# Kernel tuning notes

Hardware: AMD Instinct MI355X
Metric: run time of the kernel (lower is better)

## Reference

```python
import jax, jax.numpy as jnp
import numpy as np

EPS = 1e-5  # torch BatchNorm1d default eps


def _bn(x, gamma, beta):
    # Training-mode BatchNorm1d: per-batch mean/var (biased), affine.
    mu = jnp.mean(x, axis=0)
    var = jnp.var(x, axis=0)
    return (x - mu) * jax.lax.rsqrt(var + EPS) * gamma + beta


def _trunk(x, layers):
    # For each hidden layer: Tanh(Linear(BatchNorm(x)))
    for (W, b, g, be) in layers:
        x = jnp.tanh(_bn(x, g, be) @ W + b)
    return x


def setup_inputs() -> dict:
    key = jax.random.key(0)
    ks = jax.random.split(key, 16)
    B, N, D = 4096, 8192, 1024
    dims = [D, 1024, 512, 256]
    inp = {
        "x": jax.random.normal(ks[0], (B, D), dtype=jnp.float32),
        "x_n": jax.random.normal(ks[1], (N, D), dtype=jnp.float32),
        "y_n": jax.random.uniform(ks[2], (N, 1), dtype=jnp.float32),
    }
    for i in range(3):
        fan_in, fan_out = dims[i], dims[i + 1]
        bound = 1.0 / np.sqrt(fan_in)
        inp[f"W{i+1}"] = jax.random.uniform(ks[3 + 4 * i], (fan_in, fan_out), minval=-bound, maxval=bound, dtype=jnp.float32)
        inp[f"b{i+1}"] = jax.random.uniform(ks[4 + 4 * i], (fan_out,), minval=-bound, maxval=bound, dtype=jnp.float32)
        inp[f"g{i+1}"] = jnp.ones((fan_in,), dtype=jnp.float32)
        inp[f"beta{i+1}"] = jnp.zeros((fan_in,), dtype=jnp.float32)
    return inp


def reference(x, x_n, y_n,
              W1, b1, g1, beta1,
              W2, b2, g2, beta2,
              W3, b3, g3, beta3):
    layers = [(W1, b1, g1, beta1), (W2, b2, g2, beta2), (W3, b3, g3, beta3)]
    q = _trunk(x, layers)      # [B, 256]
    k = _trunk(x_n, layers)    # [N, 256]
    # l2 similarity: negative squared euclidean distance, via GEMM.
    # sim[i,j] = -||q_i - k_j||^2 = 2 q_i.k_j - ||q_i||^2 - ||k_j||^2
    q2 = jnp.sum(q * q, axis=1, keepdims=True)          # [B,1]
    k2 = jnp.sum(k * k, axis=1)                          # [N]
    sim = 2.0 * (q @ k.T) - q2 - k2[None, :]             # [B,N]
    # x != x_n (different shapes) => train=False, no diagonal masking.
    scores = jax.nn.softmax(sim, axis=1)
    out = jnp.clip(scores @ y_n, 0.0, 1.0)               # [B,1]
    return jnp.squeeze(out, axis=1)                      # [B]
```

## Files before the change

### kernel.cpp

```cpp
#include <hip/hip_runtime.h>
#include <math.h>
#include <stdint.h>


typedef __attribute__((ext_vector_type(8))) _Float16 half8;
typedef __attribute__((ext_vector_type(4))) _Float16 half4;
typedef __attribute__((ext_vector_type(4))) float floatx4;

#define L2E  1.4426950408889634f
#define SCALE2 2.8853901817f

__device__ __forceinline__ float fast_tanh(float x) {
    float ax = fabsf(x);
    float e  = __expf(-2.0f * ax);
    float r  = (1.0f - e) / (1.0f + e);
    return copysignf(r, x);
}
__device__ __forceinline__ void gload16(const void* g, void* l) {
    __builtin_amdgcn_global_load_lds(
        (__attribute__((address_space(1))) void*)(uintptr_t)(g),
        (__attribute__((address_space(3))) void*)(unsigned int)(uintptr_t)(l),
        16, 0, 0);
}

__global__ __launch_bounds__(256) void tof16_stats_all(
        const float* __restrict__ xn, const float* __restrict__ x,
        _Float16* __restrict__ xnh, _Float16* __restrict__ xh,
        float* __restrict__ cs0, float* __restrict__ cq0,
        float* __restrict__ cs3, float* __restrict__ cq3) {
    const float* in; _Float16* out; float *cs, *cq; int r0;
    if (blockIdx.x < 256) { in = xn; out = xnh; cs = cs0; cq = cq0; r0 = blockIdx.x * 32; }
    else                  { in = x;  out = xh;  cs = cs3; cq = cq3; r0 = (blockIdx.x - 256) * 32; }
    const int c = threadIdx.x * 4;
    float s0 = 0.f, s1 = 0.f, s2 = 0.f, s3 = 0.f;
    float q0 = 0.f, q1 = 0.f, q2 = 0.f, q3 = 0.f;
    for (int r = r0; r < r0 + 32; ++r) {
        float4 v = *(const float4*)&in[(size_t)r * 1024 + c];
        half4 h;
        h[0] = (_Float16)v.x; h[1] = (_Float16)v.y;
        h[2] = (_Float16)v.z; h[3] = (_Float16)v.w;
        *(half4*)&out[(size_t)r * 1024 + c] = h;
        s0 += v.x; q0 += v.x * v.x;
        s1 += v.y; q1 += v.y * v.y;
        s2 += v.z; q2 += v.z * v.z;
        s3 += v.w; q3 += v.w * v.w;
    }
    atomicAdd(&cs[c + 0], s0); atomicAdd(&cq[c + 0], q0);
    atomicAdd(&cs[c + 1], s1); atomicAdd(&cq[c + 1], q1);
    atomicAdd(&cs[c + 2], s2); atomicAdd(&cq[c + 2], q2);
    atomicAdd(&cs[c + 3], s3); atomicAdd(&cq[c + 3], q3);
}

__global__ __launch_bounds__(256) void wprep2(
        const float* __restrict__ W, const float* __restrict__ g,
        const float* __restrict__ beta,
        const float* __restrict__ csK, const float* __restrict__ cqK, float invRK,
        _Float16* __restrict__ WTk, float* __restrict__ baccK,
        const float* __restrict__ csQ, const float* __restrict__ cqQ, float invRQ,
        _Float16* __restrict__ WTq, float* __restrict__ baccQ,
        int C, int F) {
    const int z = blockIdx.z;
    const float* cs = z ? csQ : csK;
    const float* cq = z ? cqQ : cqK;
    const float invR = z ? invRQ : invRK;
    _Float16* WT = z ? WTq : WTk;
    float* bacc = z ? baccQ : baccK;

    __shared__ float sv[32], tv[32];
    __shared__ float tile[32][33];
    __shared__ float lds2[8][32];
    const int c0 = blockIdx.y * 32, f0 = blockIdx.x * 32;
    const int tx = threadIdx.x & 31, ty = threadIdx.x >> 5;
    if (ty == 0) {
        int c = c0 + tx;
        float mean = cs[c] * invR;
        float var  = fmaxf(cq[c] * invR - mean * mean, 0.f);
        float s    = g[c] * rsqrtf(var + 1e-5f);
        sv[tx] = s;
        tv[tx] = beta[c] - mean * s;
    }
    __syncthreads();
    float pacc = 0.f;
#pragma unroll
    for (int i = 0; i < 32; i += 8) {
        float w = W[(size_t)(c0 + ty + i) * F + f0 + tx];
        tile[ty + i][tx] = w * sv[ty + i];
        pacc += w * tv[ty + i];
    }
    lds2[ty][tx] = pacc;
    __syncthreads();
#pragma unroll
    for (int i = 0; i < 32; i += 8)
        WT[(size_t)(f0 + ty + i) * C + c0 + tx] = (_Float16)tile[tx][ty + i];
    if (ty == 0) {
        float a = 0.f;
#pragma unroll
        for (int j = 0; j < 8; ++j) a += lds2[j][tx];
        atomicAdd(&bacc[f0 + tx], a);
    }
}

__global__ __launch_bounds__(256, 4) void gemm_tn_tanh(
        const _Float16* __restrict__ Ak, const _Float16* __restrict__ Aq,
        const _Float16* __restrict__ WTk, const _Float16* __restrict__ WTq,
        const float* __restrict__ bias,
        const float* __restrict__ baccK, const float* __restrict__ baccQ,
        _Float16* __restrict__ Yk, _Float16* __restrict__ Yq,
        int K, int F, int smodeK, int smodeQ,
        float* __restrict__ csK, float* __restrict__ cqK,
        float* __restrict__ csQ, float* __restrict__ cqQ,
        float* __restrict__ rowsqK) {
    __shared__ _Float16 As[128 * 64];
    __shared__ _Float16 Bs[128 * 64];
    const int tid = threadIdx.x;
    const int wv = tid >> 6, ln = tid & 63;
    const int quad = ln >> 4, l16 = ln & 15;
    const int wr = wv >> 1, wc = wv & 1;

    const bool isK = blockIdx.x < 64;
    const _Float16* A  = isK ? Ak : Aq;
    const _Float16* WT = isK ? WTk : WTq;
    const float* bacc  = isK ? baccK : baccQ;
    _Float16* Y        = isK ? Yk : Yq;
    const int smode    = isK ? smodeK : smodeQ;
    float* cs = isK ? csK : csQ;
    float* cq = isK ? cqK : cqQ;
    const int i0 = (isK ? blockIdx.x : blockIdx.x - 64) * 128;
    const int f0 = blockIdx.y * 128;

    floatx4 acc[4][4];
#pragma unroll
    for (int a = 0; a < 4; ++a)
#pragma unroll
        for (int b = 0; b < 4; ++b) acc[a][b] = (floatx4)0.f;

    for (int k0 = 0; k0 < K; k0 += 64) {
        const char* Ab = (const char*)(A + (size_t)i0 * K + k0);
        const char* Bb = (const char*)(WT + (size_t)f0 * K + k0);
#pragma unroll
        for (int it = 0; it < 4; ++it) {
            int seg = it * 256 + tid;
            int row = seg >> 3, p = seg & 7;
            int lcol = (p ^ row) & 7;
            gload16(Ab + (size_t)row * (K * 2) + lcol * 16, (char*)As + seg * 16);
        }
#pragma unroll
        for (int it = 0; it < 4; ++it) {
            int seg = it * 256 + tid;
            int row = seg >> 3, p = seg & 7;
            int lcol = (p ^ row) & 7;
            gload16(Bb + (size_t)row * (K * 2) + lcol * 16, (char*)Bs + seg * 16);
        }
        __syncthreads();
#pragma unroll
        for (int kk = 0; kk < 2; ++kk) {
            half8 af[4], bf[4];
#pragma unroll
            for (int t = 0; t < 4; ++t) {
                int ra = wr * 64 + t * 16 + l16;
                int ca = ((kk * 4 + quad) ^ ra) & 7;
                af[t] = *(const half8*)((const char*)As + ra * 128 + ca * 16);
                int rb = wc * 64 + t * 16 + l16;
                int cb = ((kk * 4 + quad) ^ rb) & 7;
                bf[t] = *(const half8*)((const char*)Bs + rb * 128 + cb * 16);
            }
#pragma unroll
            for (int tr = 0; tr < 4; ++tr)
#pragma unroll
                for (int tc = 0; tc < 4; ++tc)
                    acc[tr][tc] = __builtin_amdgcn_mfma_f32_16x16x32_f16(af[tr], bf[tc], acc[tr][tc], 0, 0, 0);
        }
        __syncthreads();
    }
#pragma unroll
    for (int tc = 0; tc < 4; ++tc) {
        int f = f0 + wc * 64 + tc * 16 + l16;
        float bb = bias[f] + bacc[f];
#pragma unroll
        for (int tr = 0; tr < 4; ++tr)
#pragma unroll
            for (int r = 0; r < 4; ++r) {
                int row = i0 + wr * 64 + tr * 16 + quad * 4 + r;
                float v = fast_tanh(acc[tr][tc][r] + bb);
                acc[tr][tc][r] = v;
                Y[(size_t)row * F + f] = (_Float16)v;
            }
    }
    if (smode == 1) {
#pragma unroll
        for (int tc = 0; tc < 4; ++tc) {
            int f = f0 + wc * 64 + tc * 16 + l16;
            float s = 0.f, q = 0.f;
#pragma unroll
            for (int tr = 0; tr < 4; ++tr)
#pragma unroll
                for (int r = 0; r < 4; ++r) {
                    float v = acc[tr][tc][r];
                    s += v; q += v * v;
                }
            s += __shfl_xor(s, 16); q += __shfl_xor(q, 16);
            s += __shfl_xor(s, 32); q += __shfl_xor(q, 32);
            if (quad == 0) {
                atomicAdd(&cs[f], s);
                atomicAdd(&cq[f], q);
            }
        }
    } else if (smode == 2) {
#pragma unroll
        for (int tr = 0; tr < 4; ++tr)
#pragma unroll
            for (int r = 0; r < 4; ++r) {
                float rq = 0.f;
#pragma unroll
                for (int tc = 0; tc < 4; ++tc) {
                    float v = acc[tr][tc][r];
                    rq += v * v;
                }
                rq += __shfl_xor(rq, 1); rq += __shfl_xor(rq, 2);
                rq += __shfl_xor(rq, 4); rq += __shfl_xor(rq, 8);
                if (l16 == 0)
                    atomicAdd(&rowsqK[i0 + wr * 64 + tr * 16 + quad * 4 + r], rq * L2E);
            }
    }
}

__global__ __launch_bounds__(256, 2) void flash_mfma(
        const _Float16* __restrict__ Q, const _Float16* __restrict__ K3,
        const float* __restrict__ k2s, const float* __restrict__ yv,
        float* __restrict__ pm, float* __restrict__ pl, float* __restrict__ po,
        int jlen, int nsplit) {
    __shared__ _Float16 Ts[128 * 256];
    const int tid = threadIdx.x;
    const int wv = tid >> 6, ln = tid & 63;
    const int quad = ln >> 4, l16 = ln & 15;
    const int i0 = blockIdx.x * 128;
    const int jb = blockIdx.y * jlen;
    const int nch = jlen >> 6;

    auto stage64 = [&](const _Float16* src, int bufseg) {
        const char* sb = (const char*)src;
#pragma unroll
        for (int it = 0; it < 8; ++it) {
            int seg = it * 256 + tid;
            int row = seg >> 5, p = seg & 31;
            int lcol = (p & 24) | ((p ^ row) & 7);
            gload16(sb + (size_t)row * 512 + lcol * 16, (char*)Ts + (bufseg + seg) * 16);
        }
    };

    stage64(Q + (size_t)i0 * 256, 0);
    stage64(Q + (size_t)(i0 + 64) * 256, 2048);
    __syncthreads();
    half8 qf[2][8];
#pragma unroll
    for (int tr = 0; tr < 2; ++tr)
#pragma unroll
        for (int k0 = 0; k0 < 8; ++k0) {
            int row = wv * 32 + tr * 16 + l16;
            int c = k0 * 4 + quad;
            int phys = (c & 24) | ((c ^ row) & 7);
            qf[tr][k0] = *(const half8*)((const char*)Ts + row * 512 + phys * 16);
        }
    asm volatile("s_waitcnt lgkmcnt(0)" ::: "memory");
    __syncthreads();

    float mrun[2][4], lrun[2][4], orun[2][4];
#pragma unroll
    for (int tr = 0; tr < 2; ++tr)
#pragma unroll
        for (int r = 0; r < 4; ++r) { mrun[tr][r] = -INFINITY; lrun[tr][r] = 0.f; orun[tr][r] = 0.f; }

    stage64(K3 + (size_t)jb * 256, 0);
    __syncthreads();
    for (int jc = 0; jc < nch; ++jc) {
        const int j0 = jb + jc * 64;
        const int bseg = (jc & 1) * 2048;
        if (jc + 1 < nch) stage64(K3 + (size_t)(j0 + 64) * 256, 2048 - bseg);
        floatx4 acc[2][4];
#pragma unroll
        for (int a = 0; a < 2; ++a)
#pragma unroll
            for (int b = 0; b < 4; ++b) acc[a][b] = (floatx4)0.f;
#pragma unroll
        for (int k0 = 0; k0 < 8; ++k0) {
            half8 kf[4];
#pragma unroll
            for (int tc = 0; tc < 4; ++tc) {
                int row = tc * 16 + l16;
                int c = k0 * 4 + quad;
                int phys = (c & 24) | ((c ^ row) & 7);
                kf[tc] = *(const half8*)((const char*)Ts + bseg * 16 + row * 512 + phys * 16);
            }
#pragma unroll
            for (int tr = 0; tr < 2; ++tr)
#pragma unroll
                for (int tc = 0; tc < 4; ++tc)
                    acc[tr][tc] = __builtin_amdgcn_mfma_f32_16x16x32_f16(qf[tr][k0], kf[tc], acc[tr][tc], 0, 0, 0);
        }
        float k2v[4], yv4[4];
#pragma unroll
        for (int tc = 0; tc < 4; ++tc) {
            int j = j0 + tc * 16 + l16;
            k2v[tc] = k2s[j];
            yv4[tc] = yv[j];
        }
#pragma unroll
        for (int tr = 0; tr < 2; ++tr)
#pragma unroll
            for (int r = 0; r < 4; ++r) {
                float lg[4], mt = -INFINITY;
#pragma unroll
                for (int tc = 0; tc < 4; ++tc) {
                    lg[tc] = SCALE2 * acc[tr][tc][r] - k2v[tc];
                    mt = fmaxf(mt, lg[tc]);
                }
                float mnew = fmaxf(mrun[tr][r], mt);
                float sc = exp2f(mrun[tr][r] - mnew);
                float sp = 0.f, spy = 0.f;
#pragma unroll
                for (int tc = 0; tc < 4; ++tc) {
                    float p = exp2f(lg[tc] - mnew);
                    sp  += p;
                    spy += p * yv4[tc];
                }
                lrun[tr][r] = lrun[tr][r] * sc + sp;
                orun[tr][r] = orun[tr][r] * sc + spy;
                mrun[tr][r] = mnew;
            }
        __syncthreads();
    }
#pragma unroll
    for (int tr = 0; tr < 2; ++tr)
#pragma unroll
        for (int r = 0; r < 4; ++r) {
            float m = mrun[tr][r], l = lrun[tr][r], o = orun[tr][r];
#pragma unroll
            for (int s = 1; s < 16; s <<= 1) {
                float m2 = __shfl_xor(m, s);
                float l2 = __shfl_xor(l, s);
                float o2 = __shfl_xor(o, s);
                float mn = fmaxf(m, m2);
                float a = exp2f(m - mn), b = exp2f(m2 - mn);
                l = l * a + l2 * b;
                o = o * a + o2 * b;
                m = mn;
            }
            if (l16 == 0) {
                int row = i0 + wv * 32 + tr * 16 + quad * 4 + r;
                size_t idx = (size_t)row * nsplit + blockIdx.y;
                pm[idx] = m;
                pl[idx] = l;
                po[idx] = o;
            }
        }
}

__global__ void combine_k(const float* __restrict__ pm, const float* __restrict__ pl,
                          const float* __restrict__ po, float* __restrict__ out,
                          int B, int nsplit) {
    int i = blockIdx.x * blockDim.x + threadIdx.x;
    if (i >= B) return;
    float M = -INFINITY;
    for (int s = 0; s < nsplit; ++s) M = fmaxf(M, pm[(size_t)i * nsplit + s]);
    float L = 0.f, O = 0.f;
    for (int s = 0; s < nsplit; ++s) {
        float w = exp2f(pm[(size_t)i * nsplit + s] - M);
        L += pl[(size_t)i * nsplit + s] * w;
        O += po[(size_t)i * nsplit + s] * w;
    }
    float r = O / L;
    out[i] = fminf(fmaxf(r, 0.f), 1.f);
}

extern "C" void kernel_launch(void* const* d_in, const int* in_sizes, int n_in,
                              void* d_out, int out_size, void* d_ws, size_t ws_size,
                              hipStream_t stream) {
    const float* x   = (const float*)d_in[0];
    const float* x_n = (const float*)d_in[1];
    const float* y_n = (const float*)d_in[2];
    const float* Wm[3]    = {(const float*)d_in[3],  (const float*)d_in[7],  (const float*)d_in[11]};
    const float* bm[3]    = {(const float*)d_in[4],  (const float*)d_in[8],  (const float*)d_in[12]};
    const float* gm[3]    = {(const float*)d_in[5],  (const float*)d_in[9],  (const float*)d_in[13]};
    const float* betam[3] = {(const float*)d_in[6],  (const float*)d_in[10], (const float*)d_in[14]};
    (void)in_sizes; (void)n_in; (void)out_size; (void)ws_size;

    const int B = 4096, N = 8192;
    const int NSPLIT = 16;
    const size_t M1 = 1024 * 1024;

    _Float16* h0 = (_Float16*)d_ws;
    _Float16* h1 = h0 + 8 * M1;
    _Float16* h2 = h1 + 4 * M1;
    _Float16* h3 = h2 + 8 * M1;
    _Float16* WTk = h3 + 4 * M1;
    _Float16* WTq = WTk + M1;
    float* fb = (float*)(WTq + M1);
    float* csA[6], *cqA[6];
    for (int i = 0; i < 6; ++i) { csA[i] = fb + i * 2048; cqA[i] = fb + i * 2048 + 1024; }
    float* baccK[3], *baccQ[3];
    for (int i = 0; i < 3; ++i) { baccK[i] = fb + 12288 + i * 1024; baccQ[i] = fb + 15360 + i * 1024; }
    float* k2n = fb + 18432;
    const size_t zero_floats = 18432 + 8192;
    float* pm = fb + zero_floats;
    float* pl = pm + (size_t)B * NSPLIT;
    float* po = pl + (size_t)B * NSPLIT;

    _Float16* xnh = h0, *xh = h1;
    _Float16* actAk = h2, *actAq = h3;
    _Float16* actBk = h0, *actBq = h1;
    _Float16* k3 = h2, *q3 = h2 + 2 * M1;

    hipMemsetAsync(fb, 0, zero_floats * sizeof(float), stream);
    tof16_stats_all<<<384, 256, 0, stream>>>(x_n, x, xnh, xh,
                                             csA[0], cqA[0], csA[3], cqA[3]);
    const float invRK = 1.0f / (float)N, invRQ = 1.0f / (float)B;

    wprep2<<<dim3(1024 / 32, 1024 / 32, 2), 256, 0, stream>>>(
        Wm[0], gm[0], betam[0], csA[0], cqA[0], invRK, WTk, baccK[0],
        csA[3], cqA[3], invRQ, WTq, baccQ[0], 1024, 1024);
    gemm_tn_tanh<<<dim3(96, 1024 / 128), 256, 0, stream>>>(
        xnh, xh, WTk, WTq, bm[0], baccK[0], baccQ[0], actAk, actAq,
        1024, 1024, 1, 1, csA[1], cqA[1], csA[4], cqA[4], nullptr);
    wprep2<<<dim3(512 / 32, 1024 / 32, 2), 256, 0, stream>>>(
        Wm[1], gm[1], betam[1], csA[1], cqA[1], invRK, WTk, baccK[1],
        csA[4], cqA[4], invRQ, WTq, baccQ[1], 1024, 512);
    gemm_tn_tanh<<<dim3(96, 512 / 128), 256, 0, stream>>>(
        actAk, actAq, WTk, WTq, bm[1], baccK[1], baccQ[1], actBk, actBq,
        1024, 512, 1, 1, csA[2], cqA[2], csA[5], cqA[5], nullptr);
    wprep2<<<dim3(256 / 32, 512 / 32, 2), 256, 0, stream>>>(
        Wm[2], gm[2], betam[2], csA[2], cqA[2], invRK, WTk, baccK[2],
        csA[5], cqA[5], invRQ, WTq, baccQ[2], 512, 256);
    gemm_tn_tanh<<<dim3(96, 256 / 128), 256, 0, stream>>>(
        actBk, actBq, WTk, WTq, bm[2], baccK[2], baccQ[2], k3, q3,
        512, 256, 2, 0, nullptr, nullptr, nullptr, nullptr, k2n);

    flash_mfma<<<dim3(B / 128, NSPLIT), 256, 0, stream>>>(
        q3, k3, k2n, y_n, pm, pl, po, N / NSPLIT, NSPLIT);
    combine_k<<<B / 256, 256, 0, stream>>>(pm, pl, po, (float*)d_out, B, NSPLIT);
}
```

Baseline: 270.6 us.

## Double-buffer LDS tiles with K-step 32 in trunk GEMM

```diff
diff --git a/kernel.cpp b/kernel.cpp
--- a/kernel.cpp
+++ b/kernel.cpp
@@ -110,8 +110,8 @@
         float* __restrict__ csK, float* __restrict__ cqK,
         float* __restrict__ csQ, float* __restrict__ cqQ,
         float* __restrict__ rowsqK) {
-    __shared__ _Float16 As[128 * 64];
-    __shared__ _Float16 Bs[128 * 64];
+    __shared__ _Float16 As[2][128 * 32];
+    __shared__ _Float16 Bs[2][128 * 32];
     const int tid = threadIdx.x;
     const int wv = tid >> 6, ln = tid & 63;
     const int quad = ln >> 4, l16 = ln & 15;
@@ -128,48 +128,54 @@
     const int i0 = (isK ? blockIdx.x : blockIdx.x - 64) * 128;
     const int f0 = blockIdx.y * 128;
 
+    const size_t ldb = (size_t)K * 2;
+    const char* Abase = (const char*)(A + (size_t)i0 * K);
+    const char* Bbase = (const char*)(WT + (size_t)f0 * K);
+
+    auto stage = [&](const char* src, int kb, char* dst) {
+#pragma unroll
+        for (int it = 0; it < 2; ++it) {
+            int slot = it * 256 + tid;
+            int rgrp = slot >> 4;
+            int segp = (slot >> 2) & 3;
+            int rowi = slot & 3;
+            int row  = rgrp * 4 + rowi;
+            int lseg = (segp ^ rgrp) & 3;
+            gload16(src + (size_t)row * ldb + kb + lseg * 16, dst + slot * 16);
+        }
+    };
+
     floatx4 acc[4][4];
 #pragma unroll
     for (int a = 0; a < 4; ++a)
 #pragma unroll
         for (int b = 0; b < 4; ++b) acc[a][b] = (floatx4)0.f;
 
-    for (int k0 = 0; k0 < K; k0 += 64) {
-        const char* Ab = (const char*)(A + (size_t)i0 * K + k0);
-        const char* Bb = (const char*)(WT + (size_t)f0 * K + k0);
-#pragma unroll
-        for (int it = 0; it < 4; ++it) {
-            int seg = it * 256 + tid;
-            int row = seg >> 3, p = seg & 7;
-            int lcol = (p ^ row) & 7;
-            gload16(Ab + (size_t)row * (K * 2) + lcol * 16, (char*)As + seg * 16);
-        }
-#pragma unroll
-        for (int it = 0; it < 4; ++it) {
-            int seg = it * 256 + tid;
-            int row = seg >> 3, p = seg & 7;
-            int lcol = (p ^ row) & 7;
-            gload16(Bb + (size_t)row * (K * 2) + lcol * 16, (char*)Bs + seg * 16);
-        }
-        __syncthreads();
-#pragma unroll
-        for (int kk = 0; kk < 2; ++kk) {
-            half8 af[4], bf[4];
-#pragma unroll
-            for (int t = 0; t < 4; ++t) {
-                int ra = wr * 64 + t * 16 + l16;
-                int ca = ((kk * 4 + quad) ^ ra) & 7;
-                af[t] = *(const half8*)((const char*)As + ra * 128 + ca * 16);
-                int rb = wc * 64 + t * 16 + l16;
-                int cb = ((kk * 4 + quad) ^ rb) & 7;
-                bf[t] = *(const half8*)((const char*)Bs + rb * 128 + cb * 16);
-            }
-#pragma unroll
-            for (int tr = 0; tr < 4; ++tr)
-#pragma unroll
-                for (int tc = 0; tc < 4; ++tc)
-                    acc[tr][tc] = __builtin_amdgcn_mfma_f32_16x16x32_f16(af[tr], bf[tc], acc[tr][tc], 0, 0, 0);
-        }
+    const int niter = K >> 5;
+    stage(Abase, 0, (char*)As[0]);
+    stage(Bbase, 0, (char*)Bs[0]);
+    __syncthreads();
+    for (int it = 0; it < niter; ++it) {
+        const int cur = it & 1, nxt = cur ^ 1;
+        if (it + 1 < niter) {
+            stage(Abase, (it + 1) * 64, (char*)As[nxt]);
+            stage(Bbase, (it + 1) * 64, (char*)Bs[nxt]);
+        }
+        half8 af[4], bf[4];
+#pragma unroll
+        for (int t = 0; t < 4; ++t) {
+            int ra = wr * 64 + t * 16 + l16;
+            int pa = (quad ^ (ra >> 2)) & 3;
+            af[t] = *(const half8*)((const char*)As[cur] + (ra >> 2) * 256 + pa * 64 + (ra & 3) * 16);
+            int rb = wc * 64 + t * 16 + l16;
+            int pb = (quad ^ (rb >> 2)) & 3;
+            bf[t] = *(const half8*)((const char*)Bs[cur] + (rb >> 2) * 256 + pb * 64 + (rb & 3) * 16);
+        }
+#pragma unroll
+        for (int tr = 0; tr < 4; ++tr)
+#pragma unroll
+            for (int tc = 0; tc < 4; ++tc)
+                acc[tr][tc] = __builtin_amdgcn_mfma_f32_16x16x32_f16(af[tr], bf[tc], acc[tr][tc], 0, 0, 0);
         __syncthreads();
     }
 #pragma unroll
```

New measurement: 301.2 us. 1.11x slower.

## Template trunk GEMM tiles, load A fragments directly from global, prefetch B

Applied to the files above, without the earlier changes.

```diff
diff --git a/kernel.cpp b/kernel.cpp
--- a/kernel.cpp
+++ b/kernel.cpp
@@ -100,7 +100,8 @@
     }
 }
 
-__global__ __launch_bounds__(256, 4) void gemm_tn_tanh(
+template <int BM, int BN, int WC>
+__global__ __launch_bounds__(256, 3) void gemm_tn_tanh(
         const _Float16* __restrict__ Ak, const _Float16* __restrict__ Aq,
         const _Float16* __restrict__ WTk, const _Float16* __restrict__ WTq,
         const float* __restrict__ bias,
@@ -110,14 +111,18 @@
         float* __restrict__ csK, float* __restrict__ cqK,
         float* __restrict__ csQ, float* __restrict__ cqQ,
         float* __restrict__ rowsqK) {
-    __shared__ _Float16 As[128 * 64];
-    __shared__ _Float16 Bs[128 * 64];
+    constexpr int WR = 4 / WC;
+    constexpr int TR = BM / WR / 16;
+    constexpr int TC = BN / WC / 16;
+    __shared__ _Float16 Bs[BN * 64];
     const int tid = threadIdx.x;
     const int wv = tid >> 6, ln = tid & 63;
     const int quad = ln >> 4, l16 = ln & 15;
-    const int wr = wv >> 1, wc = wv & 1;
-
-    const bool isK = blockIdx.x < 64;
+    const int wr = (WC == 1) ? wv : (wv >> 1);
+    const int wc = (WC == 1) ? 0  : (wv & 1);
+
+    const int nxk = 8192 / BM;
+    const bool isK = (int)blockIdx.x < nxk;
     const _Float16* A  = isK ? Ak : Aq;
     const _Float16* WT = isK ? WTk : WTq;
     const float* bacc  = isK ? baccK : baccQ;
@@ -125,62 +130,67 @@
     const int smode    = isK ? smodeK : smodeQ;
     float* cs = isK ? csK : csQ;
     float* cq = isK ? cqK : cqQ;
-    const int i0 = (isK ? blockIdx.x : blockIdx.x - 64) * 128;
-    const int f0 = blockIdx.y * 128;
-
-    floatx4 acc[4][4];
-#pragma unroll
-    for (int a = 0; a < 4; ++a)
-#pragma unroll
-        for (int b = 0; b < 4; ++b) acc[a][b] = (floatx4)0.f;
-
-    for (int k0 = 0; k0 < K; k0 += 64) {
-        const char* Ab = (const char*)(A + (size_t)i0 * K + k0);
-        const char* Bb = (const char*)(WT + (size_t)f0 * K + k0);
-#pragma unroll
-        for (int it = 0; it < 4; ++it) {
-            int seg = it * 256 + tid;
+    const int i0 = (isK ? blockIdx.x : blockIdx.x - nxk) * BM;
+    const int f0 = blockIdx.y * BN;
+
+    const size_t ldbB = (size_t)K * 2;
+    const char* Bbase = (const char*)(WT + (size_t)f0 * K);
+    const _Float16* Awave = A + (size_t)(i0 + wr * (BM / WR)) * K;
+
+    auto stageB = [&](int kb) {
+#pragma unroll
+        for (int s = 0; s < BN / 32; ++s) {
+            int seg = s * 256 + tid;
             int row = seg >> 3, p = seg & 7;
-            int lcol = (p ^ row) & 7;
-            gload16(Ab + (size_t)row * (K * 2) + lcol * 16, (char*)As + seg * 16);
-        }
-#pragma unroll
-        for (int it = 0; it < 4; ++it) {
-            int seg = it * 256 + tid;
-            int row = seg >> 3, p = seg & 7;
-            int lcol = (p ^ row) & 7;
-            gload16(Bb + (size_t)row * (K * 2) + lcol * 16, (char*)Bs + seg * 16);
-        }
+            int lseg = (p ^ row) & 7;
+            gload16(Bbase + (size_t)row * ldbB + kb + lseg * 16, (char*)Bs + seg * 16);
+        }
+    };
+
+    floatx4 acc[TR][TC];
+#pragma unroll
+    for (int a = 0; a < TR; ++a)
+#pragma unroll
+        for (int b = 0; b < TC; ++b) acc[a][b] = (floatx4)0.f;
+
+    const int niter = K >> 6;
+    stageB(0);
+    for (int it = 0; it < niter; ++it) {
+        half8 af[2][TR];
+#pragma unroll
+        for (int kk = 0; kk < 2; ++kk)
+#pragma unroll
+            for (int t = 0; t < TR; ++t)
+                af[kk][t] = *(const half8*)(Awave + (size_t)(t * 16 + l16) * K
+                                            + it * 64 + kk * 32 + quad * 8);
         __syncthreads();
 #pragma unroll
         for (int kk = 0; kk < 2; ++kk) {
-            half8 af[4], bf[4];
-#pragma unroll
-            for (int t = 0; t < 4; ++t) {
-                int ra = wr * 64 + t * 16 + l16;
-                int ca = ((kk * 4 + quad) ^ ra) & 7;
-                af[t] = *(const half8*)((const char*)As + ra * 128 + ca * 16);
-                int rb = wc * 64 + t * 16 + l16;
+            half8 bf[TC];
+#pragma unroll
+            for (int tc = 0; tc < TC; ++tc) {
+                int rb = wc * (BN / WC) + tc * 16 + l16;
                 int cb = ((kk * 4 + quad) ^ rb) & 7;
-                bf[t] = *(const half8*)((const char*)Bs + rb * 128 + cb * 16);
-            }
-#pragma unroll
-            for (int tr = 0; tr < 4; ++tr)
-#pragma unroll
-                for (int tc = 0; tc < 4; ++tc)
-                    acc[tr][tc] = __builtin_amdgcn_mfma_f32_16x16x32_f16(af[tr], bf[tc], acc[tr][tc], 0, 0, 0);
+                bf[tc] = *(const half8*)((const char*)Bs + rb * 128 + cb * 16);
+            }
+#pragma unroll
+            for (int tr = 0; tr < TR; ++tr)
+#pragma unroll
+                for (int tc = 0; tc < TC; ++tc)
+                    acc[tr][tc] = __builtin_amdgcn_mfma_f32_16x16x32_f16(af[kk][tr], bf[tc], acc[tr][tc], 0, 0, 0);
         }
         __syncthreads();
-    }
-#pragma unroll
-    for (int tc = 0; tc < 4; ++tc) {
-        int f = f0 + wc * 64 + tc * 16 + l16;
+        if (it + 1 < niter) stageB((it + 1) * 128);
+    }
+#pragma unroll
+    for (int tc = 0; tc < TC; ++tc) {
+        int f = f0 + wc * (BN / WC) + tc * 16 + l16;
         float bb = bias[f] + bacc[f];
 #pragma unroll
-        for (int tr = 0; tr < 4; ++tr)
+        for (int tr = 0; tr < TR; ++tr)
 #pragma unroll
             for (int r = 0; r < 4; ++r) {
-                int row = i0 + wr * 64 + tr * 16 + quad * 4 + r;
+                int row = i0 + wr * (BM / WR) + tr * 16 + quad * 4 + r;
                 float v = fast_tanh(acc[tr][tc][r] + bb);
                 acc[tr][tc][r] = v;
                 Y[(size_t)row * F + f] = (_Float16)v;
@@ -188,11 +198,11 @@
     }
     if (smode == 1) {
 #pragma unroll
-        for (int tc = 0; tc < 4; ++tc) {
-            int f = f0 + wc * 64 + tc * 16 + l16;
+        for (int tc = 0; tc < TC; ++tc) {
+            int f = f0 + wc * (BN / WC) + tc * 16 + l16;
             float s = 0.f, q = 0.f;
 #pragma unroll
-            for (int tr = 0; tr < 4; ++tr)
+            for (int tr = 0; tr < TR; ++tr)
 #pragma unroll
                 for (int r = 0; r < 4; ++r) {
                     float v = acc[tr][tc][r];
@@ -207,19 +217,19 @@
         }
     } else if (smode == 2) {
 #pragma unroll
-        for (int tr = 0; tr < 4; ++tr)
+        for (int tr = 0; tr < TR; ++tr)
 #pragma unroll
             for (int r = 0; r < 4; ++r) {
                 float rq = 0.f;
 #pragma unroll
-                for (int tc = 0; tc < 4; ++tc) {
+                for (int tc = 0; tc < TC; ++tc) {
                     float v = acc[tr][tc][r];
                     rq += v * v;
                 }
                 rq += __shfl_xor(rq, 1); rq += __shfl_xor(rq, 2);
                 rq += __shfl_xor(rq, 4); rq += __shfl_xor(rq, 8);
                 if (l16 == 0)
-                    atomicAdd(&rowsqK[i0 + wr * 64 + tr * 16 + quad * 4 + r], rq * L2E);
+                    atomicAdd(&rowsqK[i0 + wr * (BM / WR) + tr * 16 + quad * 4 + r], rq * L2E);
             }
     }
 }
@@ -418,19 +428,19 @@
     wprep2<<<dim3(1024 / 32, 1024 / 32, 2), 256, 0, stream>>>(
         Wm[0], gm[0], betam[0], csA[0], cqA[0], invRK, WTk, baccK[0],
         csA[3], cqA[3], invRQ, WTq, baccQ[0], 1024, 1024);
-    gemm_tn_tanh<<<dim3(96, 1024 / 128), 256, 0, stream>>>(
+    gemm_tn_tanh<128, 128, 2><<<dim3(96, 8), 256, 0, stream>>>(
         xnh, xh, WTk, WTq, bm[0], baccK[0], baccQ[0], actAk, actAq,
         1024, 1024, 1, 1, csA[1], cqA[1], csA[4], cqA[4], nullptr);
     wprep2<<<dim3(512 / 32, 1024 / 32, 2), 256, 0, stream>>>(
         Wm[1], gm[1], betam[1], csA[1], cqA[1], invRK, WTk, baccK[1],
         csA[4], cqA[4], invRQ, WTq, baccQ[1], 1024, 512);
-    gemm_tn_tanh<<<dim3(96, 512 / 128), 256, 0, stream>>>(
+    gemm_tn_tanh<128, 64, 1><<<dim3(96, 8), 256, 0, stream>>>(
         actAk, actAq, WTk, WTq, bm[1], baccK[1], baccQ[1], actBk, actBq,
         1024, 512, 1, 1, csA[2], cqA[2], csA[5], cqA[5], nullptr);
     wprep2<<<dim3(256 / 32, 512 / 32, 2), 256, 0, stream>>>(
         Wm[2], gm[2], betam[2], csA[2], cqA[2], invRK, WTk, baccK[2],
         csA[5], cqA[5], invRQ, WTq, baccQ[2], 512, 256);
-    gemm_tn_tanh<<<dim3(96, 256 / 128), 256, 0, stream>>>(
+    gemm_tn_tanh<64, 64, 2><<<dim3(192, 4), 256, 0, stream>>>(
         actBk, actBq, WTk, WTq, bm[2], baccK[2], baccQ[2], k3, q3,
         512, 256, 2, 0, nullptr, nullptr, nullptr, nullptr, k2n);
 
```

Measured after the change: 306.1 us. 1.13x slower.

## Fuse BatchNorm affine into GEMM A-operand and transpose all weights once

Applied to the files above, without the earlier changes.

```diff
diff --git a/kernel.cpp b/kernel.cpp
--- a/kernel.cpp
+++ b/kernel.cpp
@@ -51,67 +51,43 @@
     atomicAdd(&cs[c + 3], s3); atomicAdd(&cq[c + 3], q3);
 }
 
-__global__ __launch_bounds__(256) void wprep2(
-        const float* __restrict__ W, const float* __restrict__ g,
-        const float* __restrict__ beta,
-        const float* __restrict__ csK, const float* __restrict__ cqK, float invRK,
-        _Float16* __restrict__ WTk, float* __restrict__ baccK,
-        const float* __restrict__ csQ, const float* __restrict__ cqQ, float invRQ,
-        _Float16* __restrict__ WTq, float* __restrict__ baccQ,
-        int C, int F) {
+__global__ __launch_bounds__(256) void wtrans(
+        const float* __restrict__ W0, const float* __restrict__ W1,
+        const float* __restrict__ W2,
+        _Float16* __restrict__ T0, _Float16* __restrict__ T1,
+        _Float16* __restrict__ T2) {
     const int z = blockIdx.z;
-    const float* cs = z ? csQ : csK;
-    const float* cq = z ? cqQ : cqK;
-    const float invR = z ? invRQ : invRK;
-    _Float16* WT = z ? WTq : WTk;
-    float* bacc = z ? baccQ : baccK;
-
-    __shared__ float sv[32], tv[32];
+    const float* W = z == 0 ? W0 : (z == 1 ? W1 : W2);
+    _Float16* WT   = z == 0 ? T0 : (z == 1 ? T1 : T2);
+    const int C = (z == 2) ? 512 : 1024;
+    const int F = (z == 0) ? 1024 : (z == 1 ? 512 : 256);
+    const int f0 = blockIdx.x * 32, c0 = blockIdx.y * 32;
+    if (f0 >= F || c0 >= C) return;
     __shared__ float tile[32][33];
-    __shared__ float lds2[8][32];
-    const int c0 = blockIdx.y * 32, f0 = blockIdx.x * 32;
     const int tx = threadIdx.x & 31, ty = threadIdx.x >> 5;
-    if (ty == 0) {
-        int c = c0 + tx;
-        float mean = cs[c] * invR;
-        float var  = fmaxf(cq[c] * invR - mean * mean, 0.f);
-        float s    = g[c] * rsqrtf(var + 1e-5f);
-        sv[tx] = s;
-        tv[tx] = beta[c] - mean * s;
-    }
-    __syncthreads();
-    float pacc = 0.f;
-#pragma unroll
-    for (int i = 0; i < 32; i += 8) {
-        float w = W[(size_t)(c0 + ty + i) * F + f0 + tx];
-        tile[ty + i][tx] = w * sv[ty + i];
-        pacc += w * tv[ty + i];
-    }
-    lds2[ty][tx] = pacc;
+#pragma unroll
+    for (int i = 0; i < 32; i += 8)
+        tile[ty + i][tx] = W[(size_t)(c0 + ty + i) * F + f0 + tx];
     __syncthreads();
 #pragma unroll
     for (int i = 0; i < 32; i += 8)
         WT[(size_t)(f0 + ty + i) * C + c0 + tx] = (_Float16)tile[tx][ty + i];
-    if (ty == 0) {
-        float a = 0.f;
-#pragma unroll
-        for (int j = 0; j < 8; ++j) a += lds2[j][tx];
-        atomicAdd(&bacc[f0 + tx], a);
-    }
-}
-
-__global__ __launch_bounds__(256, 4) void gemm_tn_tanh(
+}
+
+__global__ __launch_bounds__(256, 4) void gemm_bn_tanh(
         const _Float16* __restrict__ Ak, const _Float16* __restrict__ Aq,
-        const _Float16* __restrict__ WTk, const _Float16* __restrict__ WTq,
-        const float* __restrict__ bias,
-        const float* __restrict__ baccK, const float* __restrict__ baccQ,
+        const _Float16* __restrict__ WT, const float* __restrict__ bias,
+        const float* __restrict__ csK, const float* __restrict__ cqK, float invRK,
+        const float* __restrict__ csQ, const float* __restrict__ cqQ, float invRQ,
+        const float* __restrict__ g, const float* __restrict__ beta,
         _Float16* __restrict__ Yk, _Float16* __restrict__ Yq,
         int K, int F, int smodeK, int smodeQ,
-        float* __restrict__ csK, float* __restrict__ cqK,
-        float* __restrict__ csQ, float* __restrict__ cqQ,
+        float* __restrict__ csOutK, float* __restrict__ cqOutK,
+        float* __restrict__ csOutQ, float* __restrict__ cqOutQ,
         float* __restrict__ rowsqK) {
     __shared__ _Float16 As[128 * 64];
     __shared__ _Float16 Bs[128 * 64];
+    __shared__ _Float16 svh[1024], tvh[1024];
     const int tid = threadIdx.x;
     const int wv = tid >> 6, ln = tid & 63;
     const int quad = ln >> 4, l16 = ln & 15;
@@ -119,47 +95,61 @@
 
     const bool isK = blockIdx.x < 64;
     const _Float16* A  = isK ? Ak : Aq;
-    const _Float16* WT = isK ? WTk : WTq;
-    const float* bacc  = isK ? baccK : baccQ;
+    const float* cs = isK ? csK : csQ;
+    const float* cq = isK ? cqK : cqQ;
+    const float invR = isK ? invRK : invRQ;
     _Float16* Y        = isK ? Yk : Yq;
     const int smode    = isK ? smodeK : smodeQ;
-    float* cs = isK ? csK : csQ;
-    float* cq = isK ? cqK : cqQ;
+    float* csO = isK ? csOutK : csOutQ;
+    float* cqO = isK ? cqOutK : cqOutQ;
     const int i0 = (isK ? blockIdx.x : blockIdx.x - 64) * 128;
     const int f0 = blockIdx.y * 128;
 
-    floatx4 acc[4][4];
-#pragma unroll
-    for (int a = 0; a < 4; ++a)
-#pragma unroll
-        for (int b = 0; b < 4; ++b) acc[a][b] = (floatx4)0.f;
-
-    for (int k0 = 0; k0 < K; k0 += 64) {
-        const char* Ab = (const char*)(A + (size_t)i0 * K + k0);
-        const char* Bb = (const char*)(WT + (size_t)f0 * K + k0);
+    const size_t ldb = (size_t)K * 2;
+    const char* Abase = (const char*)(A + (size_t)i0 * K);
+    const char* Bbase = (const char*)(WT + (size_t)f0 * K);
+
+    auto stage = [&](const char* src, int kb, char* dst) {
 #pragma unroll
         for (int it = 0; it < 4; ++it) {
             int seg = it * 256 + tid;
             int row = seg >> 3, p = seg & 7;
             int lcol = (p ^ row) & 7;
-            gload16(Ab + (size_t)row * (K * 2) + lcol * 16, (char*)As + seg * 16);
-        }
-#pragma unroll
-        for (int it = 0; it < 4; ++it) {
-            int seg = it * 256 + tid;
-            int row = seg >> 3, p = seg & 7;
-            int lcol = (p ^ row) & 7;
-            gload16(Bb + (size_t)row * (K * 2) + lcol * 16, (char*)Bs + seg * 16);
-        }
+            gload16(src + (size_t)row * ldb + kb + lcol * 16, dst + seg * 16);
+        }
+    };
+
+    stage(Abase, 0, (char*)As);
+    stage(Bbase, 0, (char*)Bs);
+    for (int c = tid; c < K; c += 256) {
+        float mean = cs[c] * invR;
+        float var  = fmaxf(cq[c] * invR - mean * mean, 0.f);
+        float s    = g[c] * rsqrtf(var + 1e-5f);
+        svh[c] = (_Float16)s;
+        tvh[c] = (_Float16)(beta[c] - mean * s);
+    }
+
+    floatx4 acc[4][4];
+#pragma unroll
+    for (int a = 0; a < 4; ++a)
+#pragma unroll
+        for (int b = 0; b < 4; ++b) acc[a][b] = (floatx4)0.f;
+
+    const int niter = K >> 6;
+    for (int it = 0; it < niter; ++it) {
         __syncthreads();
 #pragma unroll
         for (int kk = 0; kk < 2; ++kk) {
+            const int kc = it * 64 + kk * 32 + quad * 8;
+            half8 sv8 = *(const half8*)&svh[kc];
+            half8 tv8 = *(const half8*)&tvh[kc];
             half8 af[4], bf[4];
 #pragma unroll
             for (int t = 0; t < 4; ++t) {
                 int ra = wr * 64 + t * 16 + l16;
                 int ca = ((kk * 4 + quad) ^ ra) & 7;
                 af[t] = *(const half8*)((const char*)As + ra * 128 + ca * 16);
+                af[t] = af[t] * sv8 + tv8;
                 int rb = wc * 64 + t * 16 + l16;
                 int cb = ((kk * 4 + quad) ^ rb) & 7;
                 bf[t] = *(const half8*)((const char*)Bs + rb * 128 + cb * 16);
@@ -171,11 +161,15 @@
                     acc[tr][tc] = __builtin_amdgcn_mfma_f32_16x16x32_f16(af[tr], bf[tc], acc[tr][tc], 0, 0, 0);
         }
         __syncthreads();
+        if (it + 1 < niter) {
+            stage(Abase, (it + 1) * 128, (char*)As);
+            stage(Bbase, (it + 1) * 128, (char*)Bs);
+        }
     }
 #pragma unroll
     for (int tc = 0; tc < 4; ++tc) {
         int f = f0 + wc * 64 + tc * 16 + l16;
-        float bb = bias[f] + bacc[f];
+        float bb = bias[f];
 #pragma unroll
         for (int tr = 0; tr < 4; ++tr)
 #pragma unroll
@@ -201,8 +195,8 @@
             s += __shfl_xor(s, 16); q += __shfl_xor(q, 16);
             s += __shfl_xor(s, 32); q += __shfl_xor(q, 32);
             if (quad == 0) {
-                atomicAdd(&cs[f], s);
-                atomicAdd(&cq[f], q);
+                atomicAdd(&csO[f], s);
+                atomicAdd(&cqO[f], q);
             }
         }
     } else if (smode == 2) {
@@ -392,15 +386,14 @@
     _Float16* h1 = h0 + 8 * M1;
     _Float16* h2 = h1 + 4 * M1;
     _Float16* h3 = h2 + 8 * M1;
-    _Float16* WTk = h3 + 4 * M1;
-    _Float16* WTq = WTk + M1;
-    float* fb = (float*)(WTq + M1);
+    _Float16* WT1 = h3 + 4 * M1;
+    _Float16* WT2 = WT1 + M1;
+    _Float16* WT3 = WT2 + M1 / 2;
+    float* fb = (float*)(WT3 + M1 / 8);
     float* csA[6], *cqA[6];
     for (int i = 0; i < 6; ++i) { csA[i] = fb + i * 2048; cqA[i] = fb + i * 2048 + 1024; }
-    float* baccK[3], *baccQ[3];
-    for (int i = 0; i < 3; ++i) { baccK[i] = fb + 12288 + i * 1024; baccQ[i] = fb + 15360 + i * 1024; }
-    float* k2n = fb + 18432;
-    const size_t zero_floats = 18432 + 8192;
+    float* k2n = fb + 12288;
+    const size_t zero_floats = 12288 + 8192;
     float* pm = fb + zero_floats;
     float* pl = pm + (size_t)B * NSPLIT;
     float* po = pl + (size_t)B * NSPLIT;
@@ -411,28 +404,26 @@
     _Float16* k3 = h2, *q3 = h2 + 2 * M1;
 
     hipMemsetAsync(fb, 0, zero_floats * sizeof(float), stream);
+    wtrans<<<dim3(32, 32, 3), 256, 0, stream>>>(Wm[0], Wm[1], Wm[2], WT1, WT2, WT3);
     tof16_stats_all<<<384, 256, 0, stream>>>(x_n, x, xnh, xh,
                                              csA[0], cqA[0], csA[3], cqA[3]);
     const float invRK = 1.0f / (float)N, invRQ = 1.0f / (float)B;
 
-    wprep2<<<dim3(1024 / 32, 1024 / 32, 2), 256, 0, stream>>>(
-        Wm[0], gm[0], betam[0], csA[0], cqA[0], invRK, WTk, baccK[0],
-        csA[3], cqA[3], invRQ, WTq, baccQ[0], 1024, 1024);
-    gemm_tn_tanh<<<dim3(96, 1024 / 128), 256, 0, stream>>>(
-        xnh, xh, WTk, WTq, bm[0], baccK[0], baccQ[0], actAk, actAq,
-        1024, 1024, 1, 1, csA[1], cqA[1], csA[4], cqA[4], nullptr);
-    wprep2<<<dim3(512 / 32, 1024 / 32, 2), 256, 0, stream>>>(
-        Wm[1], gm[1], betam[1], csA[1], cqA[1], invRK, WTk, baccK[1],
-        csA[4], cqA[4], invRQ, WTq, baccQ[1], 1024, 512);
-    gemm_tn_tanh<<<dim3(96, 512 / 128), 256, 0, stream>>>(
-        actAk, actAq, WTk, WTq, bm[1], baccK[1], baccQ[1], actBk, actBq,
-        1024, 512, 1, 1, csA[2], cqA[2], csA[5], cqA[5], nullptr);
-    wprep2<<<dim3(256 / 32, 512 / 32, 2), 256, 0, stream>>>(
-        Wm[2], gm[2], betam[2], csA[2], cqA[2], invRK, WTk, baccK[2],
-        csA[5], cqA[5], invRQ, WTq, baccQ[2], 512, 256);
-    gemm_tn_tanh<<<dim3(96, 256 / 128), 256, 0, stream>>>(
-        actBk, actBq, WTk, WTq, bm[2], baccK[2], baccQ[2], k3, q3,
-        512, 256, 2, 0, nullptr, nullptr, nullptr, nullptr, k2n);
+    gemm_bn_tanh<<<dim3(96, 8), 256, 0, stream>>>(
+        xnh, xh, WT1, bm[0],
+        csA[0], cqA[0], invRK, csA[3], cqA[3], invRQ, gm[0], betam[0],
+        actAk, actAq, 1024, 1024, 1, 1,
+        csA[1], cqA[1], csA[4], cqA[4], nullptr);
+    gemm_bn_tanh<<<dim3(96, 4), 256, 0, stream>>>(
+        actAk, actAq, WT2, bm[1],
+        csA[1], cqA[1], invRK, csA[4], cqA[4], invRQ, gm[1], betam[1],
+        actBk, actBq, 1024, 512, 1, 1,
+        csA[2], cqA[2], csA[5], cqA[5], nullptr);
+    gemm_bn_tanh<<<dim3(96, 2), 256, 0, stream>>>(
+        actBk, actBq, WT3, bm[2],
+        csA[2], cqA[2], invRK, csA[5], cqA[5], invRQ, gm[2], betam[2],
+        k3, q3, 512, 256, 2, 0,
+        nullptr, nullptr, nullptr, nullptr, k2n);
 
     flash_mfma<<<dim3(B / 128, NSPLIT), 256, 0, stream>>>(
         q3, k3, k2n, y_n, pm, pl, po, N / NSPLIT, NSPLIT);
```

Result: no change. 266.2 us (-1.6%).
